# Kernel optimization log

Hardware: AMD Instinct MI355X
Metric: run time of the kernel (lower is better)

## Reference

```python
import jax, jax.numpy as jnp
import numpy as np

U = 32           # user_num (nodes)
SU = 8           # num_feature_su
H = 64           # num_neuron (GRU hidden)
NC = 4           # num_classes
B = 1024         # batch
E = U * (U - 1)  # directed edges (all ordered pairs i != j)
NUM_ITER = 3

# static edge index lists, grouped by source node i in contiguous blocks of U-1
TEMP_A = np.repeat(np.arange(U), U - 1)
TEMP_B = np.concatenate([np.concatenate([np.arange(i), np.arange(i + 1, U)]) for i in range(U)])


def _lin(x, W, b):
    # Linear with W stored as [in, out]
    return x @ W + b


def _gru(x, h, Wih, Whh, bih, bhh):
    # torch.nn.GRUCell math; Wih [3H, in], Whh [3H, H]
    gi = x @ Wih.T + bih
    gh = h @ Whh.T + bhh
    ir, iz, inn = jnp.split(gi, 3, -1)
    hr, hz, hn = jnp.split(gh, 3, -1)
    r = jax.nn.sigmoid(ir + hr)
    z = jax.nn.sigmoid(iz + hz)
    n = jnp.tanh(inn + r * hn)
    return (1.0 - z) * n + z * h


def _forward(init_features, edge_weight, noise_info, hx_init, cons, x_hat_MMSE, var_MMSE,
             W1a, b1a, W2a, b2a, W2b, b2b, W2c, b2c, W3a, b3a, W3b, b3b, W3c, b3c,
             Wih, Whh, bih, bhh, W4, b4):
    ta = jnp.asarray(TEMP_A)
    tb = jnp.asarray(TEMP_B)
    edge = edge_weight[:, :, None]                          # [B,E,1]
    noise = jnp.broadcast_to(noise_info, (B, E))[:, :, None]  # repeat(1, E)
    hx = hx_init.reshape(B * U, H)
    gru_read = None
    for it in range(NUM_ITER):
        if it == 0:
            # with_mmse=True: concat MMSE estimate and variance -> 5 input feats
            x_init = jnp.concatenate([init_features, x_hat_MMSE[:, :, None], var_MMSE[:, :, None]], 2)
            nodes = _lin(x_init, W1a, b1a)                  # [B,U,SU]
        else:
            nodes = gru_read                                # [B,U,SU]
        # gather edge endpoint features + edge weight + noise
        comb = jnp.concatenate([nodes[:, ta, :], nodes[:, tb, :], edge, noise], 2)  # [B,E,2*SU+2]
        m = jax.nn.relu(_lin(comb, W2a, b2a))               # [B,E,H]
        m = jax.nn.relu(_lin(m, W2b, b2b))                  # [B,E,H/2]
        m = jax.nn.relu(_lin(m, W2c, b2c))                  # [B,E,SU]
        # segment-sum over the U-1 contiguous edges per source node
        sum_m = m.reshape(B, U, U - 1, SU).sum(2)           # [B,U,SU]
        hx = _gru(sum_m.reshape(B * U, SU), hx, Wih, Whh, bih, bhh)
        gru_read = _lin(hx.reshape(B, U, H), W4, b4)        # [B,U,SU]
    # readout: three plain linears (no activations in original forward)
    z = _lin(_lin(_lin(gru_read, W3a, b3a), W3b, b3b), W3c, b3c)  # [B,U,NC]
    return z


def setup_inputs() -> dict:
    key = jax.random.key(0)
    ks = jax.random.split(key, 20)
    rn = lambda k, shape, s=1.0: jax.random.normal(k, shape, dtype=jnp.float32) * s
    return {
        "init_features": rn(ks[0], (B, U, 3)),
        "edge_weight": rn(ks[1], (B, E)),
        "noise_info": jax.random.uniform(ks[2], (B, 1), dtype=jnp.float32),
        "hx_init": rn(ks[3], (B, U, H)),
        "cons": rn(ks[4], (NC,)),
        "x_hat_MMSE": rn(ks[5], (B, U)),
        "var_MMSE": jax.random.uniform(ks[6], (B, U), dtype=jnp.float32),
        "W1a": rn(ks[7], (5, SU), 0.3), "b1a": jnp.zeros((SU,), jnp.float32),
        "W2a": rn(ks[8], (2 * SU + 2, H), 0.2), "b2a": jnp.zeros((H,), jnp.float32),
        "W2b": rn(ks[9], (H, H // 2), 0.1), "b2b": jnp.zeros((H // 2,), jnp.float32),
        "W2c": rn(ks[10], (H // 2, SU), 0.1), "b2c": jnp.zeros((SU,), jnp.float32),
        "W3a": rn(ks[11], (SU, H), 0.2), "b3a": jnp.zeros((H,), jnp.float32),
        "W3b": rn(ks[12], (H, H // 2), 0.1), "b3b": jnp.zeros((H // 2,), jnp.float32),
        "W3c": rn(ks[13], (H // 2, NC), 0.1), "b3c": jnp.zeros((NC,), jnp.float32),
        "Wih": rn(ks[14], (3 * H, SU), 0.2), "Whh": rn(ks[15], (3 * H, H), 0.1),
        "bih": jnp.zeros((3 * H,), jnp.float32), "bhh": jnp.zeros((3 * H,), jnp.float32),
        "W4": rn(ks[16], (H, SU), 0.1), "b4": jnp.zeros((SU,), jnp.float32),
    }


def reference(init_features, edge_weight, noise_info, hx_init, cons, x_hat_MMSE, var_MMSE,
              W1a, b1a, W2a, b2a, W2b, b2b, W2c, b2c, W3a, b3a, W3b, b3b, W3c, b3c,
              Wih, Whh, bih, bhh, W4, b4):
    return _forward(init_features, edge_weight, noise_info, hx_init, cons, x_hat_MMSE, var_MMSE,
                    W1a, b1a, W2a, b2a, W2b, b2b, W2c, b2c, W3a, b3a, W3b, b3b, W3c, b3c,
                    Wih, Whh, bih, bhh, W4, b4)
```

## Files before the change

kernel.cpp:

```cpp
#include <hip/hip_runtime.h>

#define PADH 68
#define SUMP 10

typedef float v2f __attribute__((ext_vector_type(2)));

__device__ __forceinline__ v2f v2ld(const float* p) { return *(const v2f*)p; }
__device__ __forceinline__ v2f v2fma(v2f a, v2f b, v2f c) { return __builtin_elementwise_fma(a, b, c); }
__device__ __forceinline__ v2f v2max0(v2f a) { v2f z = {0.f, 0.f}; return __builtin_elementwise_max(a, z); }

__device__ __forceinline__ float sigm_(float x) { return 1.0f / (1.0f + __expf(-x)); }
__device__ __forceinline__ float tanh_(float x) {
    x = fminf(fmaxf(x, -15.0f), 15.0f);
    const float e = __expf(2.0f * x);
    return (e - 1.0f) / (e + 1.0f);
}

__global__ __launch_bounds__(512, 2) void gnn_fused(
    const float* __restrict__ init_features,
    const float* __restrict__ edge_weight,
    const float* __restrict__ noise_info,
    const float* __restrict__ hx_init,
    const float* __restrict__ x_hat,
    const float* __restrict__ var_in,
    const float* __restrict__ W1a, const float* __restrict__ b1a,
    const float* __restrict__ W2a, const float* __restrict__ b2a,
    const float* __restrict__ W2b, const float* __restrict__ b2b,
    const float* __restrict__ W2c, const float* __restrict__ c2c_unused_name_guard,
    const float* __restrict__ W3a, const float* __restrict__ b3a,
    const float* __restrict__ W3b, const float* __restrict__ b3b,
    const float* __restrict__ W3c, const float* __restrict__ b3c,
    const float* __restrict__ Wih, const float* __restrict__ Whh,
    const float* __restrict__ bih, const float* __restrict__ bhh,
    const float* __restrict__ W4,  const float* __restrict__ b4,
    float* __restrict__ out)
{
    const float* __restrict__ b2c = c2c_unused_name_guard;
    const int t  = threadIdx.x;
    const int w  = __builtin_amdgcn_readfirstlane(t >> 6);
    const int l  = t & 63;
    const int bl = l >> 5;
    const int a  = l & 31;
    const int b0 = blockIdx.x * 2;
    const int bg = b0 + bl;

    __shared__ float s_edge[1984];
    __shared__ float s_A1[64][PADH];
    __shared__ float s_B1[64][PADH];
    __shared__ float s_hx[64][PADH];
    __shared__ float s_nodes[64][8];
    __shared__ float s_sum[64][SUMP];

    for (int i = t; i < 1984; i += 512) s_edge[i] = edge_weight[(size_t)b0*992 + i];
    for (int i = t; i < 4096; i += 512) s_hx[i >> 6][i & 63] = hx_init[(size_t)b0*2048 + i];
    const float nw = noise_info[bg];
    const v2f nwp = {nw, nw};

    {
        const float* f = init_features + ((size_t)bg*32 + a)*3;
        const float xi0 = f[0], xi1 = f[1], xi2 = f[2];
        const float xi3 = x_hat[(size_t)bg*32 + a];
        const float xi4 = var_in[(size_t)bg*32 + a];
        float acc = b1a[w];
        acc = __builtin_fmaf(xi0, W1a[0*8+w], acc);
        acc = __builtin_fmaf(xi1, W1a[1*8+w], acc);
        acc = __builtin_fmaf(xi2, W1a[2*8+w], acc);
        acc = __builtin_fmaf(xi3, W1a[3*8+w], acc);
        acc = __builtin_fmaf(xi4, W1a[4*8+w], acc);
        s_nodes[l][w] = acc;
    }
    __syncthreads();

    #pragma unroll 1
    for (int it = 0; it < 3; ++it) {
        for (int i = t; i < 64*SUMP; i += 512) ((float*)s_sum)[i] = 0.0f;

        {
            float nd[8];
            *(float4*)&nd[0] = *(const float4*)&s_nodes[l][0];
            *(float4*)&nd[4] = *(const float4*)&s_nodes[l][4];
            const int h0 = w*8;
            v2f aA[4], aB[4];
            #pragma unroll
            for (int hp = 0; hp < 4; ++hp) {
                aA[hp] = v2fma(nwp, v2ld(&W2a[1088 + h0 + 2*hp]), v2ld(&b2a[h0 + 2*hp]));
                aB[hp] = (v2f){0.f, 0.f};
            }
            #pragma unroll
            for (int k = 0; k < 8; ++k) {
                const v2f ndk = {nd[k], nd[k]};
                #pragma unroll
                for (int hp = 0; hp < 4; ++hp) {
                    aA[hp] = v2fma(ndk, v2ld(&W2a[k*64     + h0 + 2*hp]), aA[hp]);
                    aB[hp] = v2fma(ndk, v2ld(&W2a[(8+k)*64 + h0 + 2*hp]), aB[hp]);
                }
            }
            #pragma unroll
            for (int hp = 0; hp < 4; ++hp) {
                *(v2f*)&s_A1[l][h0 + 2*hp] = aA[hp];
                *(v2f*)&s_B1[l][h0 + 2*hp] = aB[hp];
            }
        }
        __syncthreads();

        v2f accoutp[4];
        #pragma unroll
        for (int cp = 0; cp < 4; ++cp) accoutp[cp] = (v2f){0.f, 0.f};

        #pragma unroll 1
        for (int i = 0; i < 4; ++i) {
            const int j = w + 8*i;
            if (j < 31) {
                const int tbv = (j < a) ? j : (j + 1);
                const float ew = s_edge[bl*992 + a*31 + j];
                const v2f ewp = {ew, ew};
                v2f m2p[16];
                #pragma unroll
                for (int p = 0; p < 16; ++p) m2p[p] = v2ld(&b2b[2*p]);
                #pragma unroll 1
                for (int kb = 0; kb < 4; ++kb) {
                    v2f m1p[8];
                    #pragma unroll
                    for (int hp = 0; hp < 8; ++hp) {
                        const int h = kb*16 + 2*hp;
                        v2f tv = v2ld(&s_A1[l][h]) + v2ld(&s_B1[bl*32 + tbv][h]);
                        tv = v2fma(ewp, v2ld(&W2a[1024 + h]), tv);
                        m1p[hp] = v2max0(tv);
                    }
                    #pragma unroll
                    for (int kkp = 0; kkp < 8; ++kkp) {
                        const float* wr0 = &W2b[(kb*16 + 2*kkp)*32];
                        const v2f mlo = {m1p[kkp].x, m1p[kkp].x};
                        #pragma unroll
                        for (int p = 0; p < 16; ++p)
                            m2p[p] = v2fma(mlo, v2ld(&wr0[2*p]), m2p[p]);
                        const v2f mhi = {m1p[kkp].y, m1p[kkp].y};
                        #pragma unroll
                        for (int p = 0; p < 16; ++p)
                            m2p[p] = v2fma(mhi, v2ld(&wr0[32 + 2*p]), m2p[p]);
                    }
                }
                #pragma unroll
                for (int p = 0; p < 16; ++p) m2p[p] = v2max0(m2p[p]);
                v2f acc3[4];
                #pragma unroll
                for (int cp = 0; cp < 4; ++cp) acc3[cp] = v2ld(&b2c[2*cp]);
                #pragma unroll
                for (int p = 0; p < 16; ++p) {
                    const v2f mx = {m2p[p].x, m2p[p].x};
                    const v2f my = {m2p[p].y, m2p[p].y};
                    #pragma unroll
                    for (int cp = 0; cp < 4; ++cp) {
                        acc3[cp] = v2fma(mx, v2ld(&W2c[(2*p)*8   + 2*cp]), acc3[cp]);
                        acc3[cp] = v2fma(my, v2ld(&W2c[(2*p+1)*8 + 2*cp]), acc3[cp]);
                    }
                }
                #pragma unroll
                for (int cp = 0; cp < 4; ++cp) accoutp[cp] += v2max0(acc3[cp]);
            }
        }
        #pragma unroll
        for (int cp = 0; cp < 4; ++cp) {
            atomicAdd(&s_sum[l][2*cp],   accoutp[cp].x);
            atomicAdd(&s_sum[l][2*cp+1], accoutp[cp].y);
        }
        __syncthreads();

        v2f hp[32];
        #pragma unroll
        for (int q = 0; q < 16; ++q)
            *(float4*)&hp[2*q] = *(const float4*)&s_hx[l][q*4];
        const v2f xp0 = v2ld(&s_sum[l][0]), xp1 = v2ld(&s_sum[l][2]),
                  xp2 = v2ld(&s_sum[l][4]), xp3 = v2ld(&s_sum[l][6]);
        __syncthreads();

        #pragma unroll 1
        for (int cc = 0; cc < 8; ++cc) {
            const int c = w*8 + cc;
            v2f ar = {0.f,0.f}, az = {0.f,0.f}, an = {0.f,0.f}, ah = {0.f,0.f};
            ar = v2fma(xp0, v2ld(&Wih[c*8+0]), ar);
            ar = v2fma(xp1, v2ld(&Wih[c*8+2]), ar);
            ar = v2fma(xp2, v2ld(&Wih[c*8+4]), ar);
            ar = v2fma(xp3, v2ld(&Wih[c*8+6]), ar);
            az = v2fma(xp0, v2ld(&Wih[(64+c)*8+0]), az);
            az = v2fma(xp1, v2ld(&Wih[(64+c)*8+2]), az);
            az = v2fma(xp2, v2ld(&Wih[(64+c)*8+4]), az);
            az = v2fma(xp3, v2ld(&Wih[(64+c)*8+6]), az);
            an = v2fma(xp0, v2ld(&Wih[(128+c)*8+0]), an);
            an = v2fma(xp1, v2ld(&Wih[(128+c)*8+2]), an);
            an = v2fma(xp2, v2ld(&Wih[(128+c)*8+4]), an);
            an = v2fma(xp3, v2ld(&Wih[(128+c)*8+6]), an);
            #pragma unroll
            for (int q = 0; q < 32; ++q) {
                ar = v2fma(hp[q], v2ld(&Whh[c*64       + 2*q]), ar);
                az = v2fma(hp[q], v2ld(&Whh[(64+c)*64  + 2*q]), az);
                ah = v2fma(hp[q], v2ld(&Whh[(128+c)*64 + 2*q]), ah);
            }
            const float r0 = bih[c]     + bhh[c]     + ar.x + ar.y;
            const float z0 = bih[64+c]  + bhh[64+c]  + az.x + az.y;
            const float n0 = bih[128+c]              + an.x + an.y;
            const float nh = bhh[128+c]              + ah.x + ah.y;
            const float rr = sigm_(r0);
            const float zz = sigm_(z0);
            const float nn = tanh_(n0 + rr*nh);
            const float hold = s_hx[l][c];
            s_hx[l][c] = (1.0f - zz)*nn + zz*hold;
        }
        __syncthreads();

        {
            float acc = b4[w];
            #pragma unroll
            for (int q = 0; q < 16; ++q) {
                const float4 hv = *(const float4*)&s_hx[l][q*4];
                acc = __builtin_fmaf(hv.x, W4[(q*4+0)*8 + w], acc);
                acc = __builtin_fmaf(hv.y, W4[(q*4+1)*8 + w], acc);
                acc = __builtin_fmaf(hv.z, W4[(q*4+2)*8 + w], acc);
                acc = __builtin_fmaf(hv.w, W4[(q*4+3)*8 + w], acc);
            }
            s_nodes[l][w] = acc;
        }
        __syncthreads();
    }

    {
        float nd[8];
        *(float4*)&nd[0] = *(const float4*)&s_nodes[l][0];
        *(float4*)&nd[4] = *(const float4*)&s_nodes[l][4];
        #pragma unroll
        for (int hh = 0; hh < 8; ++hh) {
            const int hO = w*8 + hh;
            float acc = b3a[hO];
            #pragma unroll
            for (int k = 0; k < 8; ++k) acc = __builtin_fmaf(nd[k], W3a[k*64 + hO], acc);
            s_A1[l][hO] = acc;
        }
    }
    __syncthreads();
    {
        float acc[4];
        #pragma unroll
        for (int jj = 0; jj < 4; ++jj) acc[jj] = b3b[w*4 + jj];
        #pragma unroll
        for (int q = 0; q < 16; ++q) {
            const float4 v = *(const float4*)&s_A1[l][q*4];
            #pragma unroll
            for (int jj = 0; jj < 4; ++jj) {
                const int n = w*4 + jj;
                acc[jj] = __builtin_fmaf(v.x, W3b[(q*4+0)*32 + n], acc[jj]);
                acc[jj] = __builtin_fmaf(v.y, W3b[(q*4+1)*32 + n], acc[jj]);
                acc[jj] = __builtin_fmaf(v.z, W3b[(q*4+2)*32 + n], acc[jj]);
                acc[jj] = __builtin_fmaf(v.w, W3b[(q*4+3)*32 + n], acc[jj]);
            }
        }
        #pragma unroll
        for (int jj = 0; jj < 4; ++jj) s_B1[l][w*4 + jj] = acc[jj];
    }
    __syncthreads();
    if (w < 4) {
        float acc = b3c[w];
        #pragma unroll
        for (int n = 0; n < 32; ++n)
            acc = __builtin_fmaf(s_B1[l][n], W3c[n*4 + w], acc);
        out[((size_t)bg*32 + a)*4 + w] = acc;
    }
}

extern "C" void kernel_launch(void* const* d_in, const int* in_sizes, int n_in,
                              void* d_out, int out_size, void* d_ws, size_t ws_size,
                              hipStream_t stream)
{
    const float* init_features = (const float*)d_in[0];
    const float* edge_weight   = (const float*)d_in[1];
    const float* noise_info    = (const float*)d_in[2];
    const float* hx_init       = (const float*)d_in[3];
    const float* x_hat = (const float*)d_in[5];
    const float* var_i = (const float*)d_in[6];
    const float* W1a = (const float*)d_in[7];  const float* b1a = (const float*)d_in[8];
    const float* W2a = (const float*)d_in[9];  const float* b2a = (const float*)d_in[10];
    const float* W2b = (const float*)d_in[11]; const float* b2b = (const float*)d_in[12];
    const float* W2c = (const float*)d_in[13]; const float* b2c = (const float*)d_in[14];
    const float* W3a = (const float*)d_in[15]; const float* b3a = (const float*)d_in[16];
    const float* W3b = (const float*)d_in[17]; const float* b3b = (const float*)d_in[18];
    const float* W3c = (const float*)d_in[19]; const float* b3c = (const float*)d_in[20];
    const float* Wih = (const float*)d_in[21]; const float* Whh = (const float*)d_in[22];
    const float* bih = (const float*)d_in[23]; const float* bhh = (const float*)d_in[24];
    const float* W4  = (const float*)d_in[25]; const float* b4  = (const float*)d_in[26];

    gnn_fused<<<dim3(512), dim3(512), 0, stream>>>(
        init_features, edge_weight, noise_info, hx_init, x_hat, var_i,
        W1a, b1a, W2a, b2a, W2b, b2b, W2c, b2c,
        W3a, b3a, W3b, b3b, W3c, b3c,
        Wih, Whh, bih, bhh, W4, b4, (float*)d_out);
}
```

Baseline: 338.7 us.

## Compute edge-message MLP layers 2 and 3 with fp16 MFMA instead of scalar FMAs

Replaces the per-thread scalar v2 FMA evaluation of the edge MLP (64->32->8) with 16x16x32 fp16 MFMA tiles. Each wave processes 16 edges per step, and edges are remapped to a flat slot index. W2b and W2c are staged transposed in fp16 shared memory, and the layer-2 outputs go through LDS to feed the layer-3 MFMA. Per-node sums use run-length merged shared atomics. This removes the dominant VALU FMA cost but introduces fp16 precision loss and extra LDS traffic and atomics.

```diff
diff --git a/kernel.cpp b/kernel.cpp
--- a/kernel.cpp
+++ b/kernel.cpp
@@ -3,7 +3,10 @@
 #define PADH 68
 #define SUMP 10
 
-typedef float v2f __attribute__((ext_vector_type(2)));
+typedef float  v2f   __attribute__((ext_vector_type(2)));
+typedef float  f32x4 __attribute__((ext_vector_type(4)));
+typedef __fp16 f16x8 __attribute__((ext_vector_type(8)));
+typedef __fp16 f16x2 __attribute__((ext_vector_type(2)));
 
 __device__ __forceinline__ v2f v2ld(const float* p) { return *(const v2f*)p; }
 __device__ __forceinline__ v2f v2fma(v2f a, v2f b, v2f c) { return __builtin_elementwise_fma(a, b, c); }
@@ -14,6 +17,23 @@
     x = fminf(fmaxf(x, -15.0f), 15.0f);
     const float e = __expf(2.0f * x);
     return (e - 1.0f) / (e + 1.0f);
+}
+
+__device__ __forceinline__ f16x8 mk_frag(v2f m0, v2f m1, v2f m2, v2f m3) {
+    f16x2 c0 = __builtin_amdgcn_cvt_pkrtz(m0.x, m0.y);
+    f16x2 c1 = __builtin_amdgcn_cvt_pkrtz(m1.x, m1.y);
+    f16x2 c2 = __builtin_amdgcn_cvt_pkrtz(m2.x, m2.y);
+    f16x2 c3 = __builtin_amdgcn_cvt_pkrtz(m3.x, m3.y);
+    return (f16x8){c0.x, c0.y, c1.x, c1.y, c2.x, c2.y, c3.x, c3.y};
+}
+
+__device__ __forceinline__ f16x8 m1_chunk(const float* pA, const float* pB,
+                                          const float* pw, v2f ewp) {
+    v2f m0 = v2max0(v2fma(ewp, v2ld(pw + 0), v2ld(pA + 0) + v2ld(pB + 0)));
+    v2f m1 = v2max0(v2fma(ewp, v2ld(pw + 2), v2ld(pA + 2) + v2ld(pB + 2)));
+    v2f m2 = v2max0(v2fma(ewp, v2ld(pw + 4), v2ld(pA + 4) + v2ld(pB + 4)));
+    v2f m3 = v2max0(v2fma(ewp, v2ld(pw + 6), v2ld(pA + 6) + v2ld(pB + 6)));
+    return mk_frag(m0, m1, m2, m3);
 }
 
 __global__ __launch_bounds__(512, 2) void gnn_fused(
@@ -26,7 +46,7 @@
     const float* __restrict__ W1a, const float* __restrict__ b1a,
     const float* __restrict__ W2a, const float* __restrict__ b2a,
     const float* __restrict__ W2b, const float* __restrict__ b2b,
-    const float* __restrict__ W2c, const float* __restrict__ c2c_unused_name_guard,
+    const float* __restrict__ W2c, const float* __restrict__ b2c,
     const float* __restrict__ W3a, const float* __restrict__ b3a,
     const float* __restrict__ W3b, const float* __restrict__ b3b,
     const float* __restrict__ W3c, const float* __restrict__ b3c,
@@ -35,26 +55,42 @@
     const float* __restrict__ W4,  const float* __restrict__ b4,
     float* __restrict__ out)
 {
-    const float* __restrict__ b2c = c2c_unused_name_guard;
     const int t  = threadIdx.x;
     const int w  = __builtin_amdgcn_readfirstlane(t >> 6);
     const int l  = t & 63;
     const int bl = l >> 5;
     const int a  = l & 31;
+    const int lm = l & 15;
+    const int lq = l >> 4;
     const int b0 = blockIdx.x * 2;
     const int bg = b0 + bl;
 
-    __shared__ float s_edge[1984];
-    __shared__ float s_A1[64][PADH];
-    __shared__ float s_B1[64][PADH];
-    __shared__ float s_hx[64][PADH];
-    __shared__ float s_nodes[64][8];
-    __shared__ float s_sum[64][SUMP];
+    __shared__ float  s_edge[1984];
+    __shared__ float  s_A1[64][PADH];
+    __shared__ float  s_B1[64][PADH];
+    __shared__ float  s_hx[64][PADH];
+    __shared__ float  s_nodes[64][8];
+    __shared__ float  s_sum[64][SUMP];
+    __shared__ float  s_w17[64];
+    __shared__ __fp16 s_W2bT[32][64];
+    __shared__ __fp16 s_W2cT[16][32];
+    __shared__ __fp16 s_m2[8][16][40];
 
     for (int i = t; i < 1984; i += 512) s_edge[i] = edge_weight[(size_t)b0*992 + i];
     for (int i = t; i < 4096; i += 512) s_hx[i >> 6][i & 63] = hx_init[(size_t)b0*2048 + i];
+    if (t < 64) s_w17[t] = W2a[1024 + t];
+    for (int i = t; i < 2048; i += 512) {
+        const int n = i >> 6, k = i & 63;
+        s_W2bT[n][k] = (__fp16)W2b[k*32 + n];
+    }
+    if (t < 512) {
+        const int c = t >> 5, n = t & 31;
+        s_W2cT[c][n] = (c < 8) ? (__fp16)W2c[n*8 + c] : (__fp16)0.f;
+    }
     const float nw = noise_info[bg];
     const v2f nwp = {nw, nw};
+    const float b2b_l0 = b2b[lm], b2b_l1 = b2b[lm + 16];
+    const float b2c_l  = (lm < 8) ? b2c[lm] : 0.f;
 
     {
         const float* f = init_features + ((size_t)bg*32 + a)*3;
@@ -103,66 +139,69 @@
         }
         __syncthreads();
 
-        v2f accoutp[4];
-        #pragma unroll
-        for (int cp = 0; cp < 4; ++cp) accoutp[cp] = (v2f){0.f, 0.f};
-
-        #pragma unroll 1
-        for (int i = 0; i < 4; ++i) {
-            const int j = w + 8*i;
-            if (j < 31) {
-                const int tbv = (j < a) ? j : (j + 1);
-                const float ew = s_edge[bl*992 + a*31 + j];
-                const v2f ewp = {ew, ew};
-                v2f m2p[16];
+        {
+            const f16x8 Wb00 = *(const f16x8*)&s_W2bT[lm     ][     lq*8];
+            const f16x8 Wb01 = *(const f16x8*)&s_W2bT[lm     ][32 + lq*8];
+            const f16x8 Wb10 = *(const f16x8*)&s_W2bT[16 + lm][     lq*8];
+            const f16x8 Wb11 = *(const f16x8*)&s_W2bT[16 + lm][32 + lq*8];
+            const f16x8 Wcf  = *(const f16x8*)&s_W2cT[lm][lq*8];
+
+            #pragma unroll 1
+            for (int tt = 0; tt < 16; ++tt) {
+                const int slot = w*256 + tt*16 + lm;
+                const int bls  = slot >> 10;
+                const int e    = slot & 1023;
+                const bool ok  = (e < 992);
+                const int ae   = (e * 2115) >> 16;
+                const int jj   = e - ae*31;
+                const int rA   = ok ? (bls*32 + ae) : 0;
+                const int rB   = ok ? (bls*32 + ((jj < ae) ? jj : jj + 1)) : 0;
+                const float ew = ok ? s_edge[bls*992 + e] : 0.f;
+                const v2f ewp  = {ew, ew};
+
+                const f16x8 a0 = m1_chunk(&s_A1[rA][lq*8],      &s_B1[rB][lq*8],
+                                          &s_w17[lq*8],         ewp);
+                const f16x8 a1 = m1_chunk(&s_A1[rA][32 + lq*8], &s_B1[rB][32 + lq*8],
+                                          &s_w17[32 + lq*8],    ewp);
+
+                f32x4 acc0 = {0.f,0.f,0.f,0.f}, acc1 = {0.f,0.f,0.f,0.f};
+                acc0 = __builtin_amdgcn_mfma_f32_16x16x32_f16(a0, Wb00, acc0, 0, 0, 0);
+                acc0 = __builtin_amdgcn_mfma_f32_16x16x32_f16(a1, Wb01, acc0, 0, 0, 0);
+                acc1 = __builtin_amdgcn_mfma_f32_16x16x32_f16(a0, Wb10, acc1, 0, 0, 0);
+                acc1 = __builtin_amdgcn_mfma_f32_16x16x32_f16(a1, Wb11, acc1, 0, 0, 0);
+
                 #pragma unroll
-                for (int p = 0; p < 16; ++p) m2p[p] = v2ld(&b2b[2*p]);
-                #pragma unroll 1
-                for (int kb = 0; kb < 4; ++kb) {
-                    v2f m1p[8];
+                for (int r = 0; r < 4; ++r) {
+                    s_m2[w][lq*4 + r][lm]      = (__fp16)fmaxf(acc0[r] + b2b_l0, 0.f);
+                    s_m2[w][lq*4 + r][16 + lm] = (__fp16)fmaxf(acc1[r] + b2b_l1, 0.f);
+                }
+                const f16x8 a3 = *(const f16x8*)&s_m2[w][lm][lq*8];
+                f32x4 acc3 = {0.f,0.f,0.f,0.f};
+                acc3 = __builtin_amdgcn_mfma_f32_16x16x32_f16(a3, Wcf, acc3, 0, 0, 0);
+
+                if (lm < 8) {
+                    float vals[4]; int an[4];
                     #pragma unroll
-                    for (int hp = 0; hp < 8; ++hp) {
-                        const int h = kb*16 + 2*hp;
-                        v2f tv = v2ld(&s_A1[l][h]) + v2ld(&s_B1[bl*32 + tbv][h]);
-                        tv = v2fma(ewp, v2ld(&W2a[1024 + h]), tv);
-                        m1p[hp] = v2max0(tv);
+                    for (int r = 0; r < 4; ++r) {
+                        const int sl  = w*256 + tt*16 + lq*4 + r;
+                        const int bl2 = sl >> 10;
+                        const int e2  = sl & 1023;
+                        const int a2  = (e2 * 2115) >> 16;
+                        an[r]   = (e2 < 992) ? (bl2*32 + a2) : -1;
+                        vals[r] = fmaxf(acc3[r] + b2c_l, 0.f);
                     }
+                    float run = vals[0]; int ra = an[0];
                     #pragma unroll
-                    for (int kkp = 0; kkp < 8; ++kkp) {
-                        const float* wr0 = &W2b[(kb*16 + 2*kkp)*32];
-                        const v2f mlo = {m1p[kkp].x, m1p[kkp].x};
-                        #pragma unroll
-                        for (int p = 0; p < 16; ++p)
-                            m2p[p] = v2fma(mlo, v2ld(&wr0[2*p]), m2p[p]);
-                        const v2f mhi = {m1p[kkp].y, m1p[kkp].y};
-                        #pragma unroll
-                        for (int p = 0; p < 16; ++p)
-                            m2p[p] = v2fma(mhi, v2ld(&wr0[32 + 2*p]), m2p[p]);
+                    for (int r = 1; r < 4; ++r) {
+                        if (an[r] == ra) { run += vals[r]; }
+                        else {
+                            if (ra >= 0) atomicAdd(&s_sum[ra][lm], run);
+                            run = vals[r]; ra = an[r];
+                        }
                     }
+                    if (ra >= 0) atomicAdd(&s_sum[ra][lm], run);
                 }
-                #pragma unroll
-                for (int p = 0; p < 16; ++p) m2p[p] = v2max0(m2p[p]);
-                v2f acc3[4];
-                #pragma unroll
-                for (int cp = 0; cp < 4; ++cp) acc3[cp] = v2ld(&b2c[2*cp]);
-                #pragma unroll
-                for (int p = 0; p < 16; ++p) {
-                    const v2f mx = {m2p[p].x, m2p[p].x};
-                    const v2f my = {m2p[p].y, m2p[p].y};
-                    #pragma unroll
-                    for (int cp = 0; cp < 4; ++cp) {
-                        acc3[cp] = v2fma(mx, v2ld(&W2c[(2*p)*8   + 2*cp]), acc3[cp]);
-                        acc3[cp] = v2fma(my, v2ld(&W2c[(2*p+1)*8 + 2*cp]), acc3[cp]);
-                    }
-                }
-                #pragma unroll
-                for (int cp = 0; cp < 4; ++cp) accoutp[cp] += v2max0(acc3[cp]);
-            }
-        }
-        #pragma unroll
-        for (int cp = 0; cp < 4; ++cp) {
-            atomicAdd(&s_sum[l][2*cp],   accoutp[cp].x);
-            atomicAdd(&s_sum[l][2*cp+1], accoutp[cp].y);
+            }
         }
         __syncthreads();
 
```

After: 298.0 us. -12.0%, faster.
